# Performance work log

Hardware: AMD Instinct MI355X
Metric: run time of the kernel (lower is better)

## Reference

```python
import jax, jax.numpy as jnp
import numpy as np

N, D, H = 8192, 64, 128
GRID = 256
RADIUS2 = 9  # radius=3 squared


def setup_inputs() -> dict:
    key = jax.random.key(0)
    ks = jax.random.split(key, 9)
    s = lambda k, shape, scale: jax.random.normal(k, shape, dtype=jnp.float32) * scale
    return {
        "positions": jax.random.randint(ks[0], (N, 2), 0, GRID, dtype=jnp.int32),
        "states": s(ks[1], (N, D), 0.1),
        "h": s(ks[2], (N, H), 0.1),
        "c": s(ks[3], (N, H), 0.1),
        "W_ih": s(ks[4], (4 * H, 2 * D), 1.0 / np.sqrt(2 * D)),
        "W_hh": s(ks[5], (4 * H, H), 1.0 / np.sqrt(H)),
        "b": s(ks[6], (4 * H,), 0.01),
        "W_out": s(ks[7], (H, D), 1.0 / np.sqrt(H)),
        "W_role": s(ks[8], (H, 3), 1.0 / np.sqrt(H)),
    }


def reference(positions, states, h, c, W_ih, W_hh, b, W_out, W_role):
    # --- neighbor gather: all-pairs distance on integer grid, radius 3 ---
    d = positions[:, None, :] - positions[None, :, :]          # [N,N,2]
    dist2 = jnp.sum(d * d, axis=-1)                            # [N,N] int32
    mask = (dist2 <= RADIUS2) & (~jnp.eye(N, dtype=bool))      # exclude self
    maskf = mask.astype(states.dtype)
    cnt = jnp.sum(maskf, axis=1, keepdims=True)                # [N,1]
    # mean of neighbor states; zeros when no neighbors (matches zeros fallback)
    nbr_mean = (maskf @ states) / jnp.maximum(cnt, 1.0)        # [N,D]

    # --- per-cell LSTM memory update ---
    x = jnp.concatenate([states, nbr_mean], axis=-1)           # [N,2D]
    gates = x @ W_ih.T + h @ W_hh.T + b                        # [N,4H]
    i_g, f_g, g_g, o_g = jnp.split(gates, 4, axis=-1)
    c_new = jax.nn.sigmoid(f_g) * c + jax.nn.sigmoid(i_g) * jnp.tanh(g_g)
    h_new = jax.nn.sigmoid(o_g) * jnp.tanh(c_new)              # [N,H]

    new_states = h_new @ W_out                                 # [N,D]
    role_probs = jax.nn.softmax(h_new @ W_role, axis=-1)       # [N,3]
    return new_states, role_probs
```

## Files before the change

### kernel.cpp

```cpp
#include <hip/hip_runtime.h>
#include <hip/hip_bf16.h>
#include <math.h>

#define N_CELLS 8192
#define D_DIM 64
#define H_DIM 128
#define GRID_SZ 256
#define NBINS (GRID_SZ * GRID_SZ)
#define BUCKET_CAP 16

typedef short bf16x8 __attribute__((ext_vector_type(8)));
typedef float f32x4 __attribute__((ext_vector_type(4)));

static __device__ __forceinline__ short f2bf(float x) {
    __hip_bfloat16 b = __float2bfloat16(x);
    return __builtin_bit_cast(short, b);
}

__global__ __launch_bounds__(256) void prep(const float* __restrict__ Wih,
                                            const float* __restrict__ Whh,
                                            const float* __restrict__ W_out,
                                            const float* __restrict__ W_role,
                                            __hip_bfloat16* __restrict__ Wb,
                                            __hip_bfloat16* __restrict__ Wohi,
                                            __hip_bfloat16* __restrict__ Wolo,
                                            __hip_bfloat16* __restrict__ Wr,
                                            int4* __restrict__ counts4) {
    int tid = threadIdx.x, b = blockIdx.x;
    if (b < 128) {
        int idx4 = b * 256 + tid;
        int gp = idx4 >> 6, k4 = (idx4 & 63) << 2;
        int group = gp >> 6, c6 = gp & 63, gate = c6 >> 4, hl = c6 & 15;
        int orig = gate * 128 + group * 16 + hl;
        float4 v = (k4 < 128) ? *(const float4*)(Wih + orig * 128 + k4)
                              : *(const float4*)(Whh + orig * 128 + (k4 - 128));
        short4 o = make_short4(f2bf(v.x), f2bf(v.y), f2bf(v.z), f2bf(v.w));
        *(short4*)((short*)Wb + gp * 256 + k4) = o;
    } else if (b < 192) {
        counts4[(b - 128) * 256 + tid] = make_int4(0, 0, 0, 0);
    } else if (b < 224) {
        int u = (b - 192) * 256 + tid;
        int hh = u >> 6, d = u & 63;
        float w = W_out[u];
        float whi = __bfloat162float(__float2bfloat16(w));
        Wohi[d * 128 + hh] = __float2bfloat16(whi);
        Wolo[d * 128 + hh] = __float2bfloat16(w - whi);
    } else {
        #pragma unroll
        for (int e = 0; e < 8; ++e) {
            int u = e * 256 + tid;
            int r = u >> 7, hh = u & 127;
            float w = (r < 3) ? W_role[hh * 3 + r] : 0.0f;
            Wr[r * 128 + hh] = __float2bfloat16(w);
        }
    }
}

__global__ __launch_bounds__(256) void bin_fill(const int* __restrict__ positions,
                                                int* __restrict__ counts,
                                                int* __restrict__ buckets) {
    int i = blockIdx.x * 256 + threadIdx.x;
    if (i >= N_CELLS) return;
    int p0 = positions[2 * i], p1 = positions[2 * i + 1];
    int bin = p0 * GRID_SZ + p1;
    int slot = atomicAdd(&counts[bin], 1);
    if (slot < BUCKET_CAP) buckets[bin * BUCKET_CAP + slot] = i;
}

__global__ __launch_bounds__(256) void build_xh(const int* __restrict__ positions,
                                                const float* __restrict__ states,
                                                const float* __restrict__ h,
                                                const int* __restrict__ counts,
                                                const int* __restrict__ buckets,
                                                __hip_bfloat16* __restrict__ xh) {
    int wave = threadIdx.x >> 6;
    int lane = threadIdx.x & 63;
    int i = blockIdx.x * 4 + wave;
    int p0 = positions[2 * i], p1 = positions[2 * i + 1];

    int t = lane;
    int da, db;
    if (t == 0)      { da = -3; db = 0; }
    else if (t < 6)  { da = -2; db = t - 3; }
    else if (t < 11) { da = -1; db = t - 8; }
    else if (t < 18) { da = 0;  db = t - 14; }
    else if (t < 23) { da = 1;  db = t - 20; }
    else if (t < 28) { da = 2;  db = t - 25; }
    else             { da = 3;  db = 0; }

    int q0 = p0 + da, q1 = p1 + db;
    bool ok = (lane < 29) && ((unsigned)q0 < GRID_SZ) && ((unsigned)q1 < GRID_SZ);
    int bin = q0 * GRID_SZ + q1;

    int cl = 0;
    int4 jv = make_int4(0, 0, 0, 0);
    if (ok) {
        cl = counts[bin];
        jv = *(const int4*)(buckets + bin * BUCKET_CAP);
        if (cl > BUCKET_CAP) cl = BUCKET_CAP;
    }

    unsigned long long act = __ballot(cl > 0);
    float acc = 0.0f;
    int cnt = 0;
    while (act) {
        int tb = __ffsll(act) - 1;
        act &= act - 1;
        int ct = __shfl(cl, tb);
        int j0 = __shfl(jv.x, tb), j1 = __shfl(jv.y, tb);
        int j2 = __shfl(jv.z, tb), j3 = __shfl(jv.w, tb);
        if (j0 != i)           { cnt++; acc += states[j0 * D_DIM + lane]; }
        if (ct > 1 && j1 != i) { cnt++; acc += states[j1 * D_DIM + lane]; }
        if (ct > 2 && j2 != i) { cnt++; acc += states[j2 * D_DIM + lane]; }
        if (ct > 3 && j3 != i) { cnt++; acc += states[j3 * D_DIM + lane]; }
        if (ct > 4) {
            int bb = __shfl(bin, tb) * BUCKET_CAP;
            for (int s = 4; s < ct; ++s) {
                int j = buckets[bb + s];
                if (j != i) { cnt++; acc += states[j * D_DIM + lane]; }
            }
        }
    }
    float nbr = (cnt > 0) ? acc / (float)cnt : 0.0f;

    __hip_bfloat16* row = xh + (size_t)i * 256;
    row[lane]       = __float2bfloat16(states[i * D_DIM + lane]);
    row[64 + lane]  = __float2bfloat16(nbr);
    row[128 + lane] = __float2bfloat16(h[i * H_DIM + lane]);
    row[192 + lane] = __float2bfloat16(h[i * H_DIM + 64 + lane]);
}

__global__ __launch_bounds__(512) void mega(const __hip_bfloat16* __restrict__ xh,
                                            const __hip_bfloat16* __restrict__ Wb,
                                            const float* __restrict__ bias,
                                            const float* __restrict__ c_in,
                                            const __hip_bfloat16* __restrict__ Wohi,
                                            const __hip_bfloat16* __restrict__ Wolo,
                                            const __hip_bfloat16* __restrict__ Wr,
                                            float* __restrict__ out) {
    __shared__ char smem[114688];
    char* As  = smem;
    char* Bs  = smem + 4096;
    char* Whi = smem + 69632;
    char* Wlo = smem + 86016;
    char* Wrl = smem + 102400;
    char* Hl  = smem + 106496;

    const int tid  = threadIdx.x;
    const int lane = tid & 63;
    const int wid  = tid >> 6;
    const int wrow = wid >> 2, wcol = wid & 3;
    const int n0 = blockIdx.x * 32;

    const char* hiG = (const char*)Wohi;
    const char* loG = (const char*)Wolo;
    const char* wrG = (const char*)Wr;
    #pragma unroll
    for (int e = 0; e < 2; ++e) {
        int u = e * 512 + tid;
        int row = u >> 4, slot = (u & 15) << 4;
        int src = row * 256 + (slot ^ ((row & 7) << 4));
        __builtin_amdgcn_global_load_lds(
            (const __attribute__((address_space(1))) void*)(hiG + src),
            (__attribute__((address_space(3))) void*)(Whi + row * 256 + slot), 16, 0, 0);
        __builtin_amdgcn_global_load_lds(
            (const __attribute__((address_space(1))) void*)(loG + src),
            (__attribute__((address_space(3))) void*)(Wlo + row * 256 + slot), 16, 0, 0);
    }
    if (tid < 256) {
        int row = tid >> 4, slot = (tid & 15) << 4;
        __builtin_amdgcn_global_load_lds(
            (const __attribute__((address_space(1))) void*)(wrG + row * 256 + (slot ^ ((row & 7) << 4))),
            (__attribute__((address_space(3))) void*)(Wrl + row * 256 + slot), 16, 0, 0);
    }

    float cv[2][4];
    #pragma unroll
    for (int b = 0; b < 2; ++b) {
        int hg = (2 * wcol + b) * 16 + (lane & 15);
        #pragma unroll
        for (int r = 0; r < 4; ++r) {
            int ml = wrow * 16 + ((lane >> 4) << 2) + r;
            cv[b][r] = c_in[(size_t)(n0 + ml) * H_DIM + hg];
        }
    }

    const char* aG = (const char*)xh;
    const char* bG = (const char*)Wb;

    f32x4 acc[8] = {};

    for (int kc = 0; kc < 4; ++kc) {
        if (kc) __syncthreads();
        if (tid < 256) {
            int row = tid >> 3, slot = (tid & 7) << 4;
            __builtin_amdgcn_global_load_lds(
                (const __attribute__((address_space(1))) void*)(aG + (size_t)(n0 + row) * 512 + kc * 128 + (slot ^ ((row & 7) << 4))),
                (__attribute__((address_space(3))) void*)(As + row * 128 + slot), 16, 0, 0);
        }
        #pragma unroll
        for (int e = 0; e < 8; ++e) {
            int u = e * 512 + tid;
            int row = u >> 3, slot = (u & 7) << 4;
            __builtin_amdgcn_global_load_lds(
                (const __attribute__((address_space(1))) void*)(bG + (size_t)row * 512 + kc * 128 + (slot ^ ((row & 7) << 4))),
                (__attribute__((address_space(3))) void*)(Bs + row * 128 + slot), 16, 0, 0);
        }
        __syncthreads();

        #pragma unroll
        for (int ks = 0; ks < 2; ++ks) {
            int kb = ks * 64 + ((lane >> 4) << 4);
            int arow = wrow * 16 + (lane & 15);
            bf16x8 av = *(const bf16x8*)(As + arow * 128 + (kb ^ ((arow & 7) << 4)));
            #pragma unroll
            for (int ni = 0; ni < 8; ++ni) {
                int brow = wcol * 128 + ni * 16 + (lane & 15);
                bf16x8 bv = *(const bf16x8*)(Bs + brow * 128 + (kb ^ ((brow & 7) << 4)));
                acc[ni] = __builtin_amdgcn_mfma_f32_16x16x32_bf16(av, bv, acc[ni], 0, 0, 0);
            }
        }
    }

    #pragma unroll
    for (int b = 0; b < 2; ++b) {
        int hg = (2 * wcol + b) * 16 + (lane & 15);
        float bi = bias[hg], bff = bias[128 + hg], bgg = bias[256 + hg], boo = bias[384 + hg];
        #pragma unroll
        for (int r = 0; r < 4; ++r) {
            int ml = wrow * 16 + ((lane >> 4) << 2) + r;
            float ig = acc[b * 4 + 0][r] + bi;
            float fg = acc[b * 4 + 1][r] + bff;
            float gg = acc[b * 4 + 2][r] + bgg;
            float og = acc[b * 4 + 3][r] + boo;
            float si = 1.0f / (1.0f + expf(-ig));
            float sf = 1.0f / (1.0f + expf(-fg));
            float so = 1.0f / (1.0f + expf(-og));
            float hn = so * tanhf(sf * cv[b][r] + si * tanhf(gg));
            *(short*)(Hl + ml * 256 + ((hg * 2) ^ ((ml & 7) << 4))) = f2bf(hn);
        }
    }
    __syncthreads();

    const int rb = wid >> 2, db = wid & 3;
    f32x4 oacc = {};
    f32x4 racc = {};
    #pragma unroll
    for (int ks = 0; ks < 4; ++ks) {
        int kb = ks * 64 + ((lane >> 4) << 4);
        int hrow = rb * 16 + (lane & 15);
        bf16x8 hv = *(const bf16x8*)(Hl + hrow * 256 + (kb ^ ((hrow & 7) << 4)));
        int drow = db * 16 + (lane & 15);
        int woff = drow * 256 + (kb ^ ((drow & 7) << 4));
        bf16x8 whi = *(const bf16x8*)(Whi + woff);
        bf16x8 wlo = *(const bf16x8*)(Wlo + woff);
        oacc = __builtin_amdgcn_mfma_f32_16x16x32_bf16(hv, whi, oacc, 0, 0, 0);
        oacc = __builtin_amdgcn_mfma_f32_16x16x32_bf16(hv, wlo, oacc, 0, 0, 0);
        if (db == 3) {
            int rrow = lane & 15;
            bf16x8 wr = *(const bf16x8*)(Wrl + rrow * 256 + (kb ^ ((rrow & 7) << 4)));
            racc = __builtin_amdgcn_mfma_f32_16x16x32_bf16(wr, hv, racc, 0, 0, 0);
        }
    }
    #pragma unroll
    for (int r = 0; r < 4; ++r) {
        int m = n0 + rb * 16 + ((lane >> 4) << 2) + r;
        out[(size_t)m * D_DIM + db * 16 + (lane & 15)] = oacc[r];
    }
    if (db == 3 && lane < 16) {
        int m = n0 + rb * 16 + lane;
        float l0 = racc[0], l1 = racc[1], l2 = racc[2];
        float mx = fmaxf(l0, fmaxf(l1, l2));
        float e0 = expf(l0 - mx), e1 = expf(l1 - mx), e2 = expf(l2 - mx);
        float s = e0 + e1 + e2;
        float* ro = out + (size_t)N_CELLS * D_DIM + (size_t)m * 3;
        ro[0] = e0 / s; ro[1] = e1 / s; ro[2] = e2 / s;
    }
}

extern "C" void kernel_launch(void* const* d_in, const int* in_sizes, int n_in,
                              void* d_out, int out_size, void* d_ws, size_t ws_size,
                              hipStream_t stream) {
    const int*   positions = (const int*)d_in[0];
    const float* states    = (const float*)d_in[1];
    const float* h         = (const float*)d_in[2];
    const float* c         = (const float*)d_in[3];
    const float* Wih       = (const float*)d_in[4];
    const float* Whh       = (const float*)d_in[5];
    const float* bias      = (const float*)d_in[6];
    const float* Wout      = (const float*)d_in[7];
    const float* Wrole     = (const float*)d_in[8];
    float* out             = (float*)d_out;

    char* ws = (char*)d_ws;
    int*            counts  = (int*)ws;
    int*            buckets = (int*)(ws + 262144);
    __hip_bfloat16* xh      = (__hip_bfloat16*)(ws + 4456448);
    __hip_bfloat16* Wb      = (__hip_bfloat16*)(ws + 8650752);
    __hip_bfloat16* Wohi    = (__hip_bfloat16*)(ws + 8912896);
    __hip_bfloat16* Wolo    = (__hip_bfloat16*)(ws + 8929280);
    __hip_bfloat16* Wr      = (__hip_bfloat16*)(ws + 8945664);

    prep<<<225, 256, 0, stream>>>(Wih, Whh, Wout, Wrole, Wb, Wohi, Wolo, Wr, (int4*)counts);
    bin_fill<<<N_CELLS / 256, 256, 0, stream>>>(positions, counts, buckets);
    build_xh<<<N_CELLS / 4, 256, 0, stream>>>(positions, states, h, counts, buckets, xh);
    mega<<<N_CELLS / 32, 512, 0, stream>>>(xh, Wb, bias, c, Wohi, Wolo, Wr, out);
}
```

Measured before the change: 33.61 us.

## Fuse neighbor gather into LSTM GEMM kernel, build A tile in LDS

Removes the separate build_xh kernel and its global bf16 xh buffer. Each wave of the mega kernel now gathers neighbor states for four cells and writes the full 256-wide bf16 A row directly into swizzled shared memory. The first B tile is prefetched before the gather so the load overlaps it. This saves one kernel launch and a global write and read of the intermediate, at the cost of more LDS per block and serialized gather latency inside the GEMM block, which may reduce occupancy.

```diff
diff --git a/kernel.cpp b/kernel.cpp
--- a/kernel.cpp
+++ b/kernel.cpp
@@ -67,70 +67,11 @@
     if (slot < BUCKET_CAP) buckets[bin * BUCKET_CAP + slot] = i;
 }
 
-__global__ __launch_bounds__(256) void build_xh(const int* __restrict__ positions,
-                                                const float* __restrict__ states,
-                                                const float* __restrict__ h,
-                                                const int* __restrict__ counts,
-                                                const int* __restrict__ buckets,
-                                                __hip_bfloat16* __restrict__ xh) {
-    int wave = threadIdx.x >> 6;
-    int lane = threadIdx.x & 63;
-    int i = blockIdx.x * 4 + wave;
-    int p0 = positions[2 * i], p1 = positions[2 * i + 1];
-
-    int t = lane;
-    int da, db;
-    if (t == 0)      { da = -3; db = 0; }
-    else if (t < 6)  { da = -2; db = t - 3; }
-    else if (t < 11) { da = -1; db = t - 8; }
-    else if (t < 18) { da = 0;  db = t - 14; }
-    else if (t < 23) { da = 1;  db = t - 20; }
-    else if (t < 28) { da = 2;  db = t - 25; }
-    else             { da = 3;  db = 0; }
-
-    int q0 = p0 + da, q1 = p1 + db;
-    bool ok = (lane < 29) && ((unsigned)q0 < GRID_SZ) && ((unsigned)q1 < GRID_SZ);
-    int bin = q0 * GRID_SZ + q1;
-
-    int cl = 0;
-    int4 jv = make_int4(0, 0, 0, 0);
-    if (ok) {
-        cl = counts[bin];
-        jv = *(const int4*)(buckets + bin * BUCKET_CAP);
-        if (cl > BUCKET_CAP) cl = BUCKET_CAP;
-    }
-
-    unsigned long long act = __ballot(cl > 0);
-    float acc = 0.0f;
-    int cnt = 0;
-    while (act) {
-        int tb = __ffsll(act) - 1;
-        act &= act - 1;
-        int ct = __shfl(cl, tb);
-        int j0 = __shfl(jv.x, tb), j1 = __shfl(jv.y, tb);
-        int j2 = __shfl(jv.z, tb), j3 = __shfl(jv.w, tb);
-        if (j0 != i)           { cnt++; acc += states[j0 * D_DIM + lane]; }
-        if (ct > 1 && j1 != i) { cnt++; acc += states[j1 * D_DIM + lane]; }
-        if (ct > 2 && j2 != i) { cnt++; acc += states[j2 * D_DIM + lane]; }
-        if (ct > 3 && j3 != i) { cnt++; acc += states[j3 * D_DIM + lane]; }
-        if (ct > 4) {
-            int bb = __shfl(bin, tb) * BUCKET_CAP;
-            for (int s = 4; s < ct; ++s) {
-                int j = buckets[bb + s];
-                if (j != i) { cnt++; acc += states[j * D_DIM + lane]; }
-            }
-        }
-    }
-    float nbr = (cnt > 0) ? acc / (float)cnt : 0.0f;
-
-    __hip_bfloat16* row = xh + (size_t)i * 256;
-    row[lane]       = __float2bfloat16(states[i * D_DIM + lane]);
-    row[64 + lane]  = __float2bfloat16(nbr);
-    row[128 + lane] = __float2bfloat16(h[i * H_DIM + lane]);
-    row[192 + lane] = __float2bfloat16(h[i * H_DIM + 64 + lane]);
-}
-
-__global__ __launch_bounds__(512) void mega(const __hip_bfloat16* __restrict__ xh,
+__global__ __launch_bounds__(512) void mega(const int* __restrict__ positions,
+                                            const float* __restrict__ states,
+                                            const float* __restrict__ h,
+                                            const int* __restrict__ counts,
+                                            const int* __restrict__ buckets,
                                             const __hip_bfloat16* __restrict__ Wb,
                                             const float* __restrict__ bias,
                                             const float* __restrict__ c_in,
@@ -138,19 +79,32 @@
                                             const __hip_bfloat16* __restrict__ Wolo,
                                             const __hip_bfloat16* __restrict__ Wr,
                                             float* __restrict__ out) {
-    __shared__ char smem[114688];
+    __shared__ char smem[126976];
     char* As  = smem;
-    char* Bs  = smem + 4096;
-    char* Whi = smem + 69632;
-    char* Wlo = smem + 86016;
-    char* Wrl = smem + 102400;
-    char* Hl  = smem + 106496;
+    char* Bs  = smem + 16384;
+    char* Whi = smem + 81920;
+    char* Wlo = smem + 98304;
+    char* Wrl = smem + 114688;
+    char* Hl  = smem + 118784;
 
     const int tid  = threadIdx.x;
     const int lane = tid & 63;
     const int wid  = tid >> 6;
     const int wrow = wid >> 2, wcol = wid & 3;
     const int n0 = blockIdx.x * 32;
+
+    const char* bG = (const char*)Wb;
+
+    auto stageB = [&](int kcc) {
+        #pragma unroll
+        for (int e = 0; e < 8; ++e) {
+            int u = e * 512 + tid;
+            int row = u >> 3, slot = (u & 7) << 4;
+            __builtin_amdgcn_global_load_lds(
+                (const __attribute__((address_space(1))) void*)(bG + (size_t)row * 512 + kcc * 128 + (slot ^ ((row & 7) << 4))),
+                (__attribute__((address_space(3))) void*)(Bs + row * 128 + slot), 16, 0, 0);
+        }
+    };
 
     const char* hiG = (const char*)Wohi;
     const char* loG = (const char*)Wolo;
@@ -174,6 +128,8 @@
             (__attribute__((address_space(3))) void*)(Wrl + row * 256 + slot), 16, 0, 0);
     }
 
+    stageB(0);
+
     float cv[2][4];
     #pragma unroll
     for (int b = 0; b < 2; ++b) {
@@ -185,40 +141,90 @@
         }
     }
 
-    const char* aG = (const char*)xh;
-    const char* bG = (const char*)Wb;
+    {
+        int t = lane;
+        int da, db;
+        if (t == 0)      { da = -3; db = 0; }
+        else if (t < 6)  { da = -2; db = t - 3; }
+        else if (t < 11) { da = -1; db = t - 8; }
+        else if (t < 18) { da = 0;  db = t - 14; }
+        else if (t < 23) { da = 1;  db = t - 20; }
+        else if (t < 28) { da = 2;  db = t - 25; }
+        else             { da = 3;  db = 0; }
+
+        #pragma unroll
+        for (int cc = 0; cc < 4; ++cc) {
+            int ml = wid * 4 + cc;
+            int i = n0 + ml;
+            int p0 = positions[2 * i], p1 = positions[2 * i + 1];
+            int q0 = p0 + da, q1 = p1 + db;
+            bool ok = (lane < 29) && ((unsigned)q0 < GRID_SZ) && ((unsigned)q1 < GRID_SZ);
+            int bin = q0 * GRID_SZ + q1;
+
+            int cl = 0;
+            int4 jv = make_int4(0, 0, 0, 0);
+            if (ok) {
+                cl = counts[bin];
+                jv = *(const int4*)(buckets + bin * BUCKET_CAP);
+                if (cl > BUCKET_CAP) cl = BUCKET_CAP;
+            }
+
+            unsigned long long act = __ballot(cl > 0);
+            float acc = 0.0f;
+            int cnt = 0;
+            while (act) {
+                int tb = __ffsll(act) - 1;
+                act &= act - 1;
+                int ct = __shfl(cl, tb);
+                int j0 = __shfl(jv.x, tb), j1 = __shfl(jv.y, tb);
+                int j2 = __shfl(jv.z, tb), j3 = __shfl(jv.w, tb);
+                if (j0 != i)           { cnt++; acc += states[j0 * D_DIM + lane]; }
+                if (ct > 1 && j1 != i) { cnt++; acc += states[j1 * D_DIM + lane]; }
+                if (ct > 2 && j2 != i) { cnt++; acc += states[j2 * D_DIM + lane]; }
+                if (ct > 3 && j3 != i) { cnt++; acc += states[j3 * D_DIM + lane]; }
+                if (ct > 4) {
+                    int bb = __shfl(bin, tb) * BUCKET_CAP;
+                    for (int s = 4; s < ct; ++s) {
+                        int j = buckets[bb + s];
+                        if (j != i) { cnt++; acc += states[j * D_DIM + lane]; }
+                    }
+                }
+            }
+            float nbr = (cnt > 0) ? acc / (float)cnt : 0.0f;
+            float sv = states[i * D_DIM + lane];
+            float h0 = h[i * H_DIM + lane];
+            float h1 = h[i * H_DIM + 64 + lane];
+
+            int ro = ml * 512;
+            int swz = (ml & 7) << 4;
+            *(short*)(As + ro + ((2 * lane) ^ swz))       = f2bf(sv);
+            *(short*)(As + ro + ((128 + 2 * lane) ^ swz)) = f2bf(nbr);
+            *(short*)(As + ro + ((256 + 2 * lane) ^ swz)) = f2bf(h0);
+            *(short*)(As + ro + ((384 + 2 * lane) ^ swz)) = f2bf(h1);
+        }
+    }
+    __syncthreads();
 
     f32x4 acc[8] = {};
 
     for (int kc = 0; kc < 4; ++kc) {
-        if (kc) __syncthreads();
-        if (tid < 256) {
-            int row = tid >> 3, slot = (tid & 7) << 4;
-            __builtin_amdgcn_global_load_lds(
-                (const __attribute__((address_space(1))) void*)(aG + (size_t)(n0 + row) * 512 + kc * 128 + (slot ^ ((row & 7) << 4))),
-                (__attribute__((address_space(3))) void*)(As + row * 128 + slot), 16, 0, 0);
-        }
-        #pragma unroll
-        for (int e = 0; e < 8; ++e) {
-            int u = e * 512 + tid;
-            int row = u >> 3, slot = (u & 7) << 4;
-            __builtin_amdgcn_global_load_lds(
-                (const __attribute__((address_space(1))) void*)(bG + (size_t)row * 512 + kc * 128 + (slot ^ ((row & 7) << 4))),
-                (__attribute__((address_space(3))) void*)(Bs + row * 128 + slot), 16, 0, 0);
-        }
-        __syncthreads();
-
         #pragma unroll
         for (int ks = 0; ks < 2; ++ks) {
+            int arow = wrow * 16 + (lane & 15);
+            int acol = (kc * 128 + ks * 64 + ((lane >> 4) << 4)) ^ ((arow & 7) << 4);
+            bf16x8 av = *(const bf16x8*)(As + arow * 512 + acol);
             int kb = ks * 64 + ((lane >> 4) << 4);
-            int arow = wrow * 16 + (lane & 15);
-            bf16x8 av = *(const bf16x8*)(As + arow * 128 + (kb ^ ((arow & 7) << 4)));
             #pragma unroll
             for (int ni = 0; ni < 8; ++ni) {
                 int brow = wcol * 128 + ni * 16 + (lane & 15);
                 bf16x8 bv = *(const bf16x8*)(Bs + brow * 128 + (kb ^ ((brow & 7) << 4)));
                 acc[ni] = __builtin_amdgcn_mfma_f32_16x16x32_bf16(av, bv, acc[ni], 0, 0, 0);
             }
+        }
+        if (kc < 3) {
+            __syncthreads();
+            stageB(kc + 1);
+            __syncthreads();
         }
     }
 
@@ -242,7 +248,7 @@
     }
     __syncthreads();
 
-    const int rb = wid >> 2, db = wid & 3;
+    const int rb = wid >> 2, db2 = wid & 3;
     f32x4 oacc = {};
     f32x4 racc = {};
     #pragma unroll
@@ -250,13 +256,13 @@
         int kb = ks * 64 + ((lane >> 4) << 4);
         int hrow = rb * 16 + (lane & 15);
         bf16x8 hv = *(const bf16x8*)(Hl + hrow * 256 + (kb ^ ((hrow & 7) << 4)));
-        int drow = db * 16 + (lane & 15);
+        int drow = db2 * 16 + (lane & 15);
         int woff = drow * 256 + (kb ^ ((drow & 7) << 4));
         bf16x8 whi = *(const bf16x8*)(Whi + woff);
         bf16x8 wlo = *(const bf16x8*)(Wlo + woff);
         oacc = __builtin_amdgcn_mfma_f32_16x16x32_bf16(hv, whi, oacc, 0, 0, 0);
         oacc = __builtin_amdgcn_mfma_f32_16x16x32_bf16(hv, wlo, oacc, 0, 0, 0);
-        if (db == 3) {
+        if (db2 == 3) {
             int rrow = lane & 15;
             bf16x8 wr = *(const bf16x8*)(Wrl + rrow * 256 + (kb ^ ((rrow & 7) << 4)));
             racc = __builtin_amdgcn_mfma_f32_16x16x32_bf16(wr, hv, racc, 0, 0, 0);
@@ -265,9 +271,9 @@
     #pragma unroll
     for (int r = 0; r < 4; ++r) {
         int m = n0 + rb * 16 + ((lane >> 4) << 2) + r;
-        out[(size_t)m * D_DIM + db * 16 + (lane & 15)] = oacc[r];
-    }
-    if (db == 3 && lane < 16) {
+        out[(size_t)m * D_DIM + db2 * 16 + (lane & 15)] = oacc[r];
+    }
+    if (db2 == 3 && lane < 16) {
         int m = n0 + rb * 16 + lane;
         float l0 = racc[0], l1 = racc[1], l2 = racc[2];
         float mx = fmaxf(l0, fmaxf(l1, l2));
@@ -295,14 +301,13 @@
     char* ws = (char*)d_ws;
     int*            counts  = (int*)ws;
     int*            buckets = (int*)(ws + 262144);
-    __hip_bfloat16* xh      = (__hip_bfloat16*)(ws + 4456448);
-    __hip_bfloat16* Wb      = (__hip_bfloat16*)(ws + 8650752);
-    __hip_bfloat16* Wohi    = (__hip_bfloat16*)(ws + 8912896);
-    __hip_bfloat16* Wolo    = (__hip_bfloat16*)(ws + 8929280);
-    __hip_bfloat16* Wr      = (__hip_bfloat16*)(ws + 8945664);
+    __hip_bfloat16* Wb      = (__hip_bfloat16*)(ws + 4456448);
+    __hip_bfloat16* Wohi    = (__hip_bfloat16*)(ws + 4718592);
+    __hip_bfloat16* Wolo    = (__hip_bfloat16*)(ws + 4734976);
+    __hip_bfloat16* Wr      = (__hip_bfloat16*)(ws + 4751360);
 
     prep<<<225, 256, 0, stream>>>(Wih, Whh, Wout, Wrole, Wb, Wohi, Wolo, Wr, (int4*)counts);
     bin_fill<<<N_CELLS / 256, 256, 0, stream>>>(positions, counts, buckets);
-    build_xh<<<N_CELLS / 4, 256, 0, stream>>>(positions, states, h, counts, buckets, xh);
-    mega<<<N_CELLS / 32, 512, 0, stream>>>(xh, Wb, bias, c, Wohi, Wolo, Wr, out);
-}
+    mega<<<N_CELLS / 32, 512, 0, stream>>>(positions, states, h, counts, buckets,
+                                           Wb, bias, c, Wohi, Wolo, Wr, out);
+}
```

Measured after the change: 36.32 us. 1.08x slower.

## Double-buffer weight tiles and load activations straight into registers in mega kernel

Applied to the files above, without the earlier changes.

The gate GEMM now ping-pongs two LDS buffers for the weight tiles, issuing the load for the next K chunk before computing on the current one. The activation rows are read straight from global memory into registers, so the A tile no longer goes through LDS. The output and role weight loads are deferred to the last K iteration and reuse the freed weight buffer region. The bias loads move up front. This hides global-to-LDS latency behind MFMA work, at the cost of a larger LDS footprint (136 KB) and more registers.

```diff
diff --git a/kernel.cpp b/kernel.cpp
--- a/kernel.cpp
+++ b/kernel.cpp
@@ -138,13 +138,13 @@
                                             const __hip_bfloat16* __restrict__ Wolo,
                                             const __hip_bfloat16* __restrict__ Wr,
                                             float* __restrict__ out) {
-    __shared__ char smem[114688];
-    char* As  = smem;
-    char* Bs  = smem + 4096;
-    char* Whi = smem + 69632;
-    char* Wlo = smem + 86016;
-    char* Wrl = smem + 102400;
-    char* Hl  = smem + 106496;
+    __shared__ char smem[139264];
+    char* Bs0 = smem;
+    char* Bs1 = smem + 65536;
+    char* Hl  = smem + 131072;
+    char* Whi = smem;
+    char* Wlo = smem + 16384;
+    char* Wrl = smem + 32768;
 
     const int tid  = threadIdx.x;
     const int lane = tid & 63;
@@ -152,87 +152,97 @@
     const int wrow = wid >> 2, wcol = wid & 3;
     const int n0 = blockIdx.x * 32;
 
-    const char* hiG = (const char*)Wohi;
-    const char* loG = (const char*)Wolo;
-    const char* wrG = (const char*)Wr;
-    #pragma unroll
-    for (int e = 0; e < 2; ++e) {
-        int u = e * 512 + tid;
-        int row = u >> 4, slot = (u & 15) << 4;
-        int src = row * 256 + (slot ^ ((row & 7) << 4));
-        __builtin_amdgcn_global_load_lds(
-            (const __attribute__((address_space(1))) void*)(hiG + src),
-            (__attribute__((address_space(3))) void*)(Whi + row * 256 + slot), 16, 0, 0);
-        __builtin_amdgcn_global_load_lds(
-            (const __attribute__((address_space(1))) void*)(loG + src),
-            (__attribute__((address_space(3))) void*)(Wlo + row * 256 + slot), 16, 0, 0);
-    }
-    if (tid < 256) {
-        int row = tid >> 4, slot = (tid & 15) << 4;
-        __builtin_amdgcn_global_load_lds(
-            (const __attribute__((address_space(1))) void*)(wrG + row * 256 + (slot ^ ((row & 7) << 4))),
-            (__attribute__((address_space(3))) void*)(Wrl + row * 256 + slot), 16, 0, 0);
-    }
-
-    float cv[2][4];
-    #pragma unroll
-    for (int b = 0; b < 2; ++b) {
-        int hg = (2 * wcol + b) * 16 + (lane & 15);
-        #pragma unroll
-        for (int r = 0; r < 4; ++r) {
-            int ml = wrow * 16 + ((lane >> 4) << 2) + r;
-            cv[b][r] = c_in[(size_t)(n0 + ml) * H_DIM + hg];
-        }
-    }
-
-    const char* aG = (const char*)xh;
     const char* bG = (const char*)Wb;
 
-    f32x4 acc[8] = {};
-
-    for (int kc = 0; kc < 4; ++kc) {
-        if (kc) __syncthreads();
-        if (tid < 256) {
-            int row = tid >> 3, slot = (tid & 7) << 4;
-            __builtin_amdgcn_global_load_lds(
-                (const __attribute__((address_space(1))) void*)(aG + (size_t)(n0 + row) * 512 + kc * 128 + (slot ^ ((row & 7) << 4))),
-                (__attribute__((address_space(3))) void*)(As + row * 128 + slot), 16, 0, 0);
-        }
+    auto stageB = [&](int kcc, char* dst) {
         #pragma unroll
         for (int e = 0; e < 8; ++e) {
             int u = e * 512 + tid;
             int row = u >> 3, slot = (u & 7) << 4;
             __builtin_amdgcn_global_load_lds(
-                (const __attribute__((address_space(1))) void*)(bG + (size_t)row * 512 + kc * 128 + (slot ^ ((row & 7) << 4))),
-                (__attribute__((address_space(3))) void*)(Bs + row * 128 + slot), 16, 0, 0);
-        }
-        __syncthreads();
-
+                (const __attribute__((address_space(1))) void*)(bG + (size_t)row * 512 + kcc * 128 + (slot ^ ((row & 7) << 4))),
+                (__attribute__((address_space(3))) void*)(dst + row * 128 + slot), 16, 0, 0);
+        }
+    };
+
+    stageB(0, Bs0);
+
+    const short* xr = (const short*)xh + (size_t)(n0 + wrow * 16 + (lane & 15)) * 256 + ((lane >> 4) << 3);
+    bf16x8 av[8];
+    #pragma unroll
+    for (int z = 0; z < 8; ++z) av[z] = *(const bf16x8*)(xr + z * 32);
+
+    float cv[2][4];
+    float bi[2], bff[2], bgg[2], boo[2];
+    #pragma unroll
+    for (int b = 0; b < 2; ++b) {
+        int hg = (2 * wcol + b) * 16 + (lane & 15);
+        bi[b]  = bias[hg];
+        bff[b] = bias[128 + hg];
+        bgg[b] = bias[256 + hg];
+        boo[b] = bias[384 + hg];
+        #pragma unroll
+        for (int r = 0; r < 4; ++r) {
+            int ml = wrow * 16 + ((lane >> 4) << 2) + r;
+            cv[b][r] = c_in[(size_t)(n0 + ml) * H_DIM + hg];
+        }
+    }
+    __syncthreads();
+
+    f32x4 acc[8] = {};
+
+    #pragma unroll
+    for (int kc = 0; kc < 4; ++kc) {
+        if (kc < 3) {
+            stageB(kc + 1, (kc & 1) ? Bs0 : Bs1);
+        } else {
+            const char* hiG = (const char*)Wohi;
+            const char* loG = (const char*)Wolo;
+            const char* wrG = (const char*)Wr;
+            #pragma unroll
+            for (int e = 0; e < 2; ++e) {
+                int u = e * 512 + tid;
+                int row = u >> 4, slot = (u & 15) << 4;
+                int src = row * 256 + (slot ^ ((row & 7) << 4));
+                __builtin_amdgcn_global_load_lds(
+                    (const __attribute__((address_space(1))) void*)(hiG + src),
+                    (__attribute__((address_space(3))) void*)(Whi + row * 256 + slot), 16, 0, 0);
+                __builtin_amdgcn_global_load_lds(
+                    (const __attribute__((address_space(1))) void*)(loG + src),
+                    (__attribute__((address_space(3))) void*)(Wlo + row * 256 + slot), 16, 0, 0);
+            }
+            if (tid < 256) {
+                int row = tid >> 4, slot = (tid & 15) << 4;
+                __builtin_amdgcn_global_load_lds(
+                    (const __attribute__((address_space(1))) void*)(wrG + row * 256 + (slot ^ ((row & 7) << 4))),
+                    (__attribute__((address_space(3))) void*)(Wrl + row * 256 + slot), 16, 0, 0);
+            }
+        }
+
+        const char* B = (kc & 1) ? Bs1 : Bs0;
         #pragma unroll
         for (int ks = 0; ks < 2; ++ks) {
             int kb = ks * 64 + ((lane >> 4) << 4);
-            int arow = wrow * 16 + (lane & 15);
-            bf16x8 av = *(const bf16x8*)(As + arow * 128 + (kb ^ ((arow & 7) << 4)));
             #pragma unroll
             for (int ni = 0; ni < 8; ++ni) {
                 int brow = wcol * 128 + ni * 16 + (lane & 15);
-                bf16x8 bv = *(const bf16x8*)(Bs + brow * 128 + (kb ^ ((brow & 7) << 4)));
-                acc[ni] = __builtin_amdgcn_mfma_f32_16x16x32_bf16(av, bv, acc[ni], 0, 0, 0);
+                bf16x8 bv = *(const bf16x8*)(B + brow * 128 + (kb ^ ((brow & 7) << 4)));
+                acc[ni] = __builtin_amdgcn_mfma_f32_16x16x32_bf16(av[kc * 2 + ks], bv, acc[ni], 0, 0, 0);
             }
         }
+        __syncthreads();
     }
 
     #pragma unroll
     for (int b = 0; b < 2; ++b) {
         int hg = (2 * wcol + b) * 16 + (lane & 15);
-        float bi = bias[hg], bff = bias[128 + hg], bgg = bias[256 + hg], boo = bias[384 + hg];
         #pragma unroll
         for (int r = 0; r < 4; ++r) {
             int ml = wrow * 16 + ((lane >> 4) << 2) + r;
-            float ig = acc[b * 4 + 0][r] + bi;
-            float fg = acc[b * 4 + 1][r] + bff;
-            float gg = acc[b * 4 + 2][r] + bgg;
-            float og = acc[b * 4 + 3][r] + boo;
+            float ig = acc[b * 4 + 0][r] + bi[b];
+            float fg = acc[b * 4 + 1][r] + bff[b];
+            float gg = acc[b * 4 + 2][r] + bgg[b];
+            float og = acc[b * 4 + 3][r] + boo[b];
             float si = 1.0f / (1.0f + expf(-ig));
             float sf = 1.0f / (1.0f + expf(-fg));
             float so = 1.0f / (1.0f + expf(-og));
@@ -242,7 +252,7 @@
     }
     __syncthreads();
 
-    const int rb = wid >> 2, db = wid & 3;
+    const int rb = wid >> 2, db2 = wid & 3;
     f32x4 oacc = {};
     f32x4 racc = {};
     #pragma unroll
@@ -250,13 +260,13 @@
         int kb = ks * 64 + ((lane >> 4) << 4);
         int hrow = rb * 16 + (lane & 15);
         bf16x8 hv = *(const bf16x8*)(Hl + hrow * 256 + (kb ^ ((hrow & 7) << 4)));
-        int drow = db * 16 + (lane & 15);
+        int drow = db2 * 16 + (lane & 15);
         int woff = drow * 256 + (kb ^ ((drow & 7) << 4));
         bf16x8 whi = *(const bf16x8*)(Whi + woff);
         bf16x8 wlo = *(const bf16x8*)(Wlo + woff);
         oacc = __builtin_amdgcn_mfma_f32_16x16x32_bf16(hv, whi, oacc, 0, 0, 0);
         oacc = __builtin_amdgcn_mfma_f32_16x16x32_bf16(hv, wlo, oacc, 0, 0, 0);
-        if (db == 3) {
+        if (db2 == 3) {
             int rrow = lane & 15;
             bf16x8 wr = *(const bf16x8*)(Wrl + rrow * 256 + (kb ^ ((rrow & 7) << 4)));
             racc = __builtin_amdgcn_mfma_f32_16x16x32_bf16(wr, hv, racc, 0, 0, 0);
@@ -265,9 +275,9 @@
     #pragma unroll
     for (int r = 0; r < 4; ++r) {
         int m = n0 + rb * 16 + ((lane >> 4) << 2) + r;
-        out[(size_t)m * D_DIM + db * 16 + (lane & 15)] = oacc[r];
-    }
-    if (db == 3 && lane < 16) {
+        out[(size_t)m * D_DIM + db2 * 16 + (lane & 15)] = oacc[r];
+    }
+    if (db2 == 3 && lane < 16) {
         int m = n0 + rb * 16 + lane;
         float l0 = racc[0], l1 = racc[1], l2 = racc[2];
         float mx = fmaxf(l0, fmaxf(l1, l2));
@@ -304,5 +314,5 @@
     prep<<<225, 256, 0, stream>>>(Wih, Whh, Wout, Wrole, Wb, Wohi, Wolo, Wr, (int4*)counts);
     bin_fill<<<N_CELLS / 256, 256, 0, stream>>>(positions, counts, buckets);
     build_xh<<<N_CELLS / 4, 256, 0, stream>>>(positions, states, h, counts, buckets, xh);
-    mega<<<N_CELLS / 32, 512, 0, stream>>>(xh, Wb, bias, c, Wohi, Wolo, Wr, out);
-}
+    mega<<<256, 512, 0, stream>>>(xh, Wb, bias, c, Wohi, Wolo, Wr, out);
+}
```

Result: no change. 33.61 us (+0.0%).
